# Optimization experiments

Measured on AMD Instinct MI355X. Metric: run time of the kernel, lower is better.

The kernel has to match this reference:

```python
import jax, jax.numpy as jnp
import numpy as np

N_STAGES = 400
N_CLASSES = 10          # trees per stage (dimension)
DEPTH = 6               # complete binary trees: 63 internal nodes, 64 leaves
N_TREES = N_STAGES * N_CLASSES
N_INTERNAL = 2 ** DEPTH - 1
N_LEAVES = 2 ** DEPTH
N_FEATURES = 128
BATCH = 32768
LEARNING_RATE = 0.1


def setup_inputs() -> dict:
    key = jax.random.key(0)
    k1, k2, k3, k4, k5 = jax.random.split(key, 5)
    x = jax.random.normal(k1, (BATCH, N_FEATURES), dtype=jnp.float32)
    features = jax.random.randint(k2, (N_TREES, N_INTERNAL), 0, N_FEATURES, dtype=jnp.int32)
    thresholds = jax.random.normal(k3, (N_TREES, N_INTERNAL), dtype=jnp.float32)
    leaf_values = jax.random.normal(k4, (N_TREES, N_LEAVES), dtype=jnp.float32) * 0.1
    init_out = jax.random.normal(k5, (N_CLASSES,), dtype=jnp.float32)
    return {"x": x, "features": features, "thresholds": thresholds,
            "leaf_values": leaf_values, "init_out": init_out}


def reference(x, features, thresholds, leaf_values, init_out):
    # Batched evaluation of all trees of all boosting stages at once
    # (fused form of: out = init + lr * sum_stages stack([tree(x) for tree in stage])).
    N = x.shape[0]
    T = features.shape[0]
    t_idx = jnp.arange(T)[None, :]                       # [1, T]
    idx = jnp.zeros((N, T), dtype=jnp.int32)             # current node per (sample, tree)
    for _ in range(DEPTH):
        f = features[t_idx, idx]                         # [N, T] feature id at node
        thr = thresholds[t_idx, idx]                     # [N, T]
        xv = jnp.take_along_axis(x, f, axis=1)           # [N, T] feature value
        # left child if x <= thr, right child otherwise (sklearn convention)
        idx = 2 * idx + 1 + (xv > thr).astype(jnp.int32)
    leaf = idx - N_INTERNAL                              # [N, T] leaf index
    vals = leaf_values[t_idx, leaf]                      # [N, T] raw tree outputs
    per_stage = vals.reshape(N, N_STAGES, N_CLASSES)     # [N, S, K]
    out = init_out[None, :] + LEARNING_RATE * per_stage.sum(axis=1)  # [N, K]
    return out
```

## Files before the change

### kernel.cpp

```cpp
#include <hip/hip_runtime.h>
#include <stdint.h>

#define N_CLASSES  10
#define N_TREES    4000
#define DEPTH      6
#define N_INTERNAL 63
#define N_FEATURES 128
#define BATCH      32768
#define LR         0.1f

#define BLOCK       256
#define SAMPLES_PB  32
#define TSPLIT      2
#define SLOTS_PB    (N_TREES / TSPLIT)
#define T_TILE      16
#define N_TILES     (SLOTS_PB / T_TILE)
#define TILES_PER_CLASS 25
#define NODE_DW     128
#define SUMS_STRIDE 11

#define WS_NODES_BYTES  ((size_t)N_TREES * NODE_DW * 4)
#define WS_LEAVES_BYTES ((size_t)N_TREES * 64 * 4)

__global__ void pack_kernel(const int* __restrict__ features,
                            const float* __restrict__ thresholds,
                            const float* __restrict__ leaves,
                            int* __restrict__ pn, float* __restrict__ pl) {
    int i = blockIdx.x * blockDim.x + threadIdx.x;
    int t = i >> 6, n = i & 63;
    if (t < N_TREES) {
        int slot = (t % N_CLASSES) * (N_TREES / N_CLASSES) + (t / N_CLASSES);
        if (n < N_INTERNAL) {
            pn[slot * NODE_DW + n]      = features[t * N_INTERNAL + n];
            pn[slot * NODE_DW + 64 + n] = __float_as_int(thresholds[t * N_INTERNAL + n]);
        }
        pl[slot * 64 + n] = leaves[t * 64 + n];
    }
}

__global__ void out_init_kernel(const float* __restrict__ init_out,
                                float* __restrict__ out) {
    int i = blockIdx.x * blockDim.x + threadIdx.x;
    if (i < BATCH * N_CLASSES) {
        int s = i / N_CLASSES;
        out[i] = init_out[i - s * N_CLASSES];
    }
}

__device__ __forceinline__ void load_lds_16(const void* g, void* l) {
    const auto* g1 = reinterpret_cast<const __attribute__((address_space(1))) uint32_t*>(
        reinterpret_cast<uintptr_t>(g));
    auto* l3 = reinterpret_cast<__attribute__((address_space(3))) uint32_t*>(
        reinterpret_cast<uintptr_t>(l));
    __builtin_amdgcn_global_load_lds(g1, l3, 16, 0, 0);
}

__global__ __launch_bounds__(BLOCK, 4) void gbt_eval(
    const float* __restrict__ x,
    const int*   __restrict__ pnodes,
    const float* __restrict__ pleaves,
    float*       __restrict__ out)
{
    __shared__ float xs[N_FEATURES * SAMPLES_PB];
    __shared__ int   nbuf[2][T_TILE * NODE_DW];
    __shared__ float sums[SAMPLES_PB * SUMS_STRIDE];

    const int tid = threadIdx.x;
    const int sample0 = blockIdx.x * SAMPLES_PB;
    const int slot0   = blockIdx.y * SLOTS_PB;
    const int cls0    = blockIdx.y * (N_CLASSES / TSPLIT);

    {
        const float4* xg = (const float4*)(x + (size_t)sample0 * N_FEATURES);
        for (int e = tid; e < SAMPLES_PB * (N_FEATURES / 4); e += BLOCK) {
            int s = e >> 5, f4 = e & 31;
            float4 v = xg[e];
            int f = f4 << 2;
            xs[(f + 0) * SAMPLES_PB + s] = v.x;
            xs[(f + 1) * SAMPLES_PB + s] = v.y;
            xs[(f + 2) * SAMPLES_PB + s] = v.z;
            xs[(f + 3) * SAMPLES_PB + s] = v.w;
        }
    }
    for (int i = tid; i < SAMPLES_PB * SUMS_STRIDE; i += BLOCK) sums[i] = 0.f;

    const int lane = tid & 63;
    const int wv   = tid >> 6;

    auto stage = [&](int tile, int b) {
        const char* g = (const char*)(pnodes + (size_t)(slot0 + tile * T_TILE) * NODE_DW);
        char* lbase = (char*)&nbuf[b][0];
        #pragma unroll
        for (int q = 0; q < 2; ++q) {
            int k = wv * 2 + q;
            load_lds_16(g + k * 1024 + lane * 16, lbase + k * 1024);
        }
    };

    stage(0, 0);
    __syncthreads();

    const int sLocal = tid & (SAMPLES_PB - 1);
    const int j      = tid >> 5;

    int cur = 0;
    for (int c5 = 0; c5 < N_CLASSES / TSPLIT; ++c5) {
        float acc = 0.f;
        for (int t25 = 0; t25 < TILES_PER_CLASS; ++t25) {
            const int tile = c5 * TILES_PER_CLASS + t25;
            if (tile + 1 < N_TILES) stage(tile + 1, cur ^ 1);

            const int* nb = &nbuf[cur][j * 2 * NODE_DW];
            int o0 = 0, o1 = 0;
            #pragma unroll
            for (int d = 0; d < DEPTH; ++d) {
                int   f0 = nb[o0];
                float h0 = __int_as_float(nb[o0 + 64]);
                int   f1 = nb[NODE_DW + o1];
                float h1 = __int_as_float(nb[NODE_DW + o1 + 64]);
                float x0 = xs[f0 * SAMPLES_PB + sLocal];
                float x1 = xs[f1 * SAMPLES_PB + sLocal];
                o0 = 2 * o0 + 1 + (x0 > h0 ? 1 : 0);
                o1 = 2 * o1 + 1 + (x1 > h1 ? 1 : 0);
            }
            const size_t slotA = (size_t)(slot0 + tile * T_TILE + j * 2);
            acc += pleaves[slotA * 64       + (o0 - N_INTERNAL)];
            acc += pleaves[(slotA + 1) * 64 + (o1 - N_INTERNAL)];

            __syncthreads();
            cur ^= 1;
        }
        atomicAdd(&sums[sLocal * SUMS_STRIDE + cls0 + c5], acc);
    }
    __syncthreads();

    for (int e = tid; e < SAMPLES_PB * N_CLASSES; e += BLOCK) {
        int s = e / N_CLASSES, k = e - s * N_CLASSES;
        atomicAdd(&out[(size_t)(sample0 + s) * N_CLASSES + k],
                  LR * sums[s * SUMS_STRIDE + k]);
    }
}

__global__ __launch_bounds__(BLOCK, 8) void gbt_eval_global(
    const float* __restrict__ x,
    const int*   __restrict__ features,
    const float* __restrict__ thresholds,
    const float* __restrict__ leaf_values,
    float*       __restrict__ out)
{
    __shared__ float xs[N_FEATURES * SAMPLES_PB];
    __shared__ float sums[SAMPLES_PB * N_CLASSES];
    const int tid = threadIdx.x;
    const int sample0 = blockIdx.x * SAMPLES_PB;
    {
        const float4* xg = (const float4*)(x + (size_t)sample0 * N_FEATURES);
        for (int e = tid; e < SAMPLES_PB * (N_FEATURES / 4); e += BLOCK) {
            int s = e >> 5, f4 = e & 31;
            float4 v = xg[e];
            int f = f4 << 2;
            xs[(f + 0) * SAMPLES_PB + s] = v.x;
            xs[(f + 1) * SAMPLES_PB + s] = v.y;
            xs[(f + 2) * SAMPLES_PB + s] = v.z;
            xs[(f + 3) * SAMPLES_PB + s] = v.w;
        }
    }
    for (int i = tid; i < SAMPLES_PB * N_CLASSES; i += BLOCK) sums[i] = 0.f;
    __syncthreads();
    const int sLocal = tid & (SAMPLES_PB - 1);
    const int j = tid >> 5;
    const int TPT = N_TREES / (8 * TSPLIT);
    const int t0 = (blockIdx.y * 8 + j) * TPT;
    float acc[N_CLASSES];
    #pragma unroll
    for (int k = 0; k < N_CLASSES; ++k) acc[k] = 0.f;
    for (int i = 0; i < TPT; i += N_CLASSES) {
        const int tt = t0 + i;
        int idx[N_CLASSES];
        #pragma unroll
        for (int u = 0; u < N_CLASSES; ++u) idx[u] = 0;
        #pragma unroll
        for (int d = 0; d < DEPTH; ++d) {
            #pragma unroll
            for (int u = 0; u < N_CLASSES; ++u) {
                int base = (tt + u) * N_INTERNAL + idx[u];
                float xv = xs[features[base] * SAMPLES_PB + sLocal];
                idx[u] = 2 * idx[u] + 1 + (xv > thresholds[base] ? 1 : 0);
            }
        }
        #pragma unroll
        for (int u = 0; u < N_CLASSES; ++u)
            acc[u] += leaf_values[(size_t)(tt + u) * 64 + idx[u] - N_INTERNAL];
    }
    #pragma unroll
    for (int k = 0; k < N_CLASSES; ++k)
        atomicAdd(&sums[sLocal * N_CLASSES + k], acc[k]);
    __syncthreads();
    for (int e = tid; e < SAMPLES_PB * N_CLASSES; e += BLOCK) {
        int s = e / N_CLASSES, k = e - s * N_CLASSES;
        atomicAdd(&out[(size_t)(sample0 + s) * N_CLASSES + k], LR * sums[e]);
    }
}

extern "C" void kernel_launch(void* const* d_in, const int* in_sizes, int n_in,
                              void* d_out, int out_size, void* d_ws, size_t ws_size,
                              hipStream_t stream) {
    const float* x          = (const float*)d_in[0];
    const int*   features   = (const int*)d_in[1];
    const float* thresholds = (const float*)d_in[2];
    const float* leafvals   = (const float*)d_in[3];
    const float* init_out   = (const float*)d_in[4];
    float*       out        = (float*)d_out;

    {
        int n = BATCH * N_CLASSES;
        out_init_kernel<<<(n + 255) / 256, 256, 0, stream>>>(init_out, out);
    }

    dim3 grid(BATCH / SAMPLES_PB, TSPLIT);

    if (ws_size >= WS_NODES_BYTES + WS_LEAVES_BYTES) {
        int*   pn = (int*)d_ws;
        float* pl = (float*)((char*)d_ws + WS_NODES_BYTES);
        int n = N_TREES * 64;
        pack_kernel<<<(n + 255) / 256, 256, 0, stream>>>(features, thresholds,
                                                         leafvals, pn, pl);
        gbt_eval<<<grid, BLOCK, 0, stream>>>(x, pn, pl, out);
    } else {
        gbt_eval_global<<<grid, BLOCK, 0, stream>>>(x, features, thresholds,
                                                    leafvals, out);
    }
}
```

Before: 335.2 us.

## Interleave feature/threshold pairs and split trees between LDS and global reads

Packs each node's feature id and threshold together as an int2 so one load fetches both. Only half of each 16-tree tile (8 trees) is staged into LDS; each thread walks one tree from LDS and reads the other tree's nodes directly from global memory through the cache. This halves LDS staging traffic and LDS footprint, and may improve occupancy, at the cost of dependent global loads inside the depth loop. Those loads can add latency to the traversal.

```diff
diff --git a/kernel.cpp b/kernel.cpp
--- a/kernel.cpp
+++ b/kernel.cpp
@@ -14,26 +14,25 @@
 #define TSPLIT      2
 #define SLOTS_PB    (N_TREES / TSPLIT)
 #define T_TILE      16
+#define LDS_TREES   8
 #define N_TILES     (SLOTS_PB / T_TILE)
 #define TILES_PER_CLASS 25
-#define NODE_DW     128
 #define SUMS_STRIDE 11
 
-#define WS_NODES_BYTES  ((size_t)N_TREES * NODE_DW * 4)
+#define WS_NODES_BYTES  ((size_t)N_TREES * 64 * 8)
 #define WS_LEAVES_BYTES ((size_t)N_TREES * 64 * 4)
 
 __global__ void pack_kernel(const int* __restrict__ features,
                             const float* __restrict__ thresholds,
                             const float* __restrict__ leaves,
-                            int* __restrict__ pn, float* __restrict__ pl) {
+                            int2* __restrict__ pn, float* __restrict__ pl) {
     int i = blockIdx.x * blockDim.x + threadIdx.x;
     int t = i >> 6, n = i & 63;
     if (t < N_TREES) {
         int slot = (t % N_CLASSES) * (N_TREES / N_CLASSES) + (t / N_CLASSES);
-        if (n < N_INTERNAL) {
-            pn[slot * NODE_DW + n]      = features[t * N_INTERNAL + n];
-            pn[slot * NODE_DW + 64 + n] = __float_as_int(thresholds[t * N_INTERNAL + n]);
-        }
+        if (n < N_INTERNAL)
+            pn[slot * 64 + n] = make_int2(features[t * N_INTERNAL + n],
+                                          __float_as_int(thresholds[t * N_INTERNAL + n]));
         pl[slot * 64 + n] = leaves[t * 64 + n];
     }
 }
@@ -57,12 +56,12 @@
 
 __global__ __launch_bounds__(BLOCK, 4) void gbt_eval(
     const float* __restrict__ x,
-    const int*   __restrict__ pnodes,
+    const int2*  __restrict__ pnodes,
     const float* __restrict__ pleaves,
     float*       __restrict__ out)
 {
     __shared__ float xs[N_FEATURES * SAMPLES_PB];
-    __shared__ int   nbuf[2][T_TILE * NODE_DW];
+    __shared__ int2  nbuf[2][LDS_TREES * 64];
     __shared__ float sums[SAMPLES_PB * SUMS_STRIDE];
 
     const int tid = threadIdx.x;
@@ -88,13 +87,9 @@
     const int wv   = tid >> 6;
 
     auto stage = [&](int tile, int b) {
-        const char* g = (const char*)(pnodes + (size_t)(slot0 + tile * T_TILE) * NODE_DW);
-        char* lbase = (char*)&nbuf[b][0];
-        #pragma unroll
-        for (int q = 0; q < 2; ++q) {
-            int k = wv * 2 + q;
-            load_lds_16(g + k * 1024 + lane * 16, lbase + k * 1024);
-        }
+        const char* g = (const char*)(pnodes + (size_t)(slot0 + tile * T_TILE) * 64);
+        char* l = (char*)&nbuf[b][0];
+        load_lds_16(g + wv * 1024 + lane * 16, l + wv * 1024);
     };
 
     stage(0, 0);
@@ -110,22 +105,23 @@
             const int tile = c5 * TILES_PER_CLASS + t25;
             if (tile + 1 < N_TILES) stage(tile + 1, cur ^ 1);
 
-            const int* nb = &nbuf[cur][j * 2 * NODE_DW];
+            const int2* nb = &nbuf[cur][j * 64];
+            const size_t gslot = (size_t)(slot0 + tile * T_TILE + LDS_TREES + j);
+            const int2* gp = pnodes + gslot * 64;
+
             int o0 = 0, o1 = 0;
             #pragma unroll
             for (int d = 0; d < DEPTH; ++d) {
-                int   f0 = nb[o0];
-                float h0 = __int_as_float(nb[o0 + 64]);
-                int   f1 = nb[NODE_DW + o1];
-                float h1 = __int_as_float(nb[NODE_DW + o1 + 64]);
-                float x0 = xs[f0 * SAMPLES_PB + sLocal];
-                float x1 = xs[f1 * SAMPLES_PB + sLocal];
-                o0 = 2 * o0 + 1 + (x0 > h0 ? 1 : 0);
-                o1 = 2 * o1 + 1 + (x1 > h1 ? 1 : 0);
+                int2 a = nb[o0];
+                int2 b = gp[o1];
+                float x0 = xs[a.x * SAMPLES_PB + sLocal];
+                float x1 = xs[b.x * SAMPLES_PB + sLocal];
+                o0 = 2 * o0 + 1 + (x0 > __int_as_float(a.y) ? 1 : 0);
+                o1 = 2 * o1 + 1 + (x1 > __int_as_float(b.y) ? 1 : 0);
             }
-            const size_t slotA = (size_t)(slot0 + tile * T_TILE + j * 2);
-            acc += pleaves[slotA * 64       + (o0 - N_INTERNAL)];
-            acc += pleaves[(slotA + 1) * 64 + (o1 - N_INTERNAL)];
+            const size_t lslot = (size_t)(slot0 + tile * T_TILE + j);
+            acc += pleaves[lslot * 64 + (o0 - N_INTERNAL)];
+            acc += pleaves[gslot * 64 + (o1 - N_INTERNAL)];
 
             __syncthreads();
             cur ^= 1;
@@ -219,7 +215,7 @@
     dim3 grid(BATCH / SAMPLES_PB, TSPLIT);
 
     if (ws_size >= WS_NODES_BYTES + WS_LEAVES_BYTES) {
-        int*   pn = (int*)d_ws;
+        int2*  pn = (int2*)d_ws;
         float* pl = (float*)((char*)d_ws + WS_NODES_BYTES);
         int n = N_TREES * 64;
         pack_kernel<<<(n + 255) / 256, 256, 0, stream>>>(features, thresholds,
```

Result: slower. 451.7 us (+34.7%).
